# Optimization experiments

Measured on AMD Instinct MI355X. Metric: run time of the kernel, lower is better.

Reference implementation:

```python
import jax, jax.numpy as jnp
import numpy as np

EPS = 1e-6
ROPE_THETA = 10000.0


def setup_inputs() -> dict:
    key = jax.random.key(0)
    ks = jax.random.split(key, 6)
    B, S, D = 2, 2048, 2048
    H, KVH, HD = 16, 4, 128
    hidden_states = jax.random.normal(ks[0], (B, S, D), dtype=jnp.float32)
    # RoPE tables (HF style: freqs duplicated across the two halves)
    inv_freq = 1.0 / (ROPE_THETA ** (jnp.arange(0, HD, 2, dtype=jnp.float32) / HD))
    pos = jnp.arange(S, dtype=jnp.float32)
    freqs = pos[:, None] * inv_freq[None, :]            # [S, HD/2]
    emb = jnp.concatenate([freqs, freqs], axis=-1)       # [S, HD]
    cos, sin = jnp.cos(emb), jnp.sin(emb)
    w_scale = 0.02
    q_w = jax.random.normal(ks[1], (H * HD, D), dtype=jnp.float32) * w_scale
    k_w = jax.random.normal(ks[2], (KVH * HD, D), dtype=jnp.float32) * w_scale
    v_w = jax.random.normal(ks[3], (KVH * HD, D), dtype=jnp.float32) * w_scale
    o_w = jax.random.normal(ks[4], (D, H * HD), dtype=jnp.float32) * w_scale
    q_norm_w = jnp.ones((HD,), dtype=jnp.float32)
    k_norm_w = jnp.ones((HD,), dtype=jnp.float32)
    return {
        "hidden_states": hidden_states, "cos": cos, "sin": sin,
        "q_w": q_w, "k_w": k_w, "v_w": v_w, "o_w": o_w,
        "q_norm_w": q_norm_w, "k_norm_w": k_norm_w,
    }


def _rms_norm(x, w):
    # Qwen3RMSNorm: fp32 variance, scale, cast back
    xf = x.astype(jnp.float32)
    var = jnp.mean(xf * xf, axis=-1, keepdims=True)
    out = xf * jax.lax.rsqrt(var + EPS)
    return (out * w.astype(jnp.float32)).astype(x.dtype)


def _rotate_half(x):
    half = x.shape[-1] // 2
    return jnp.concatenate([-x[..., half:], x[..., :half]], axis=-1)


def reference(hidden_states, cos, sin, q_w, k_w, v_w, o_w, q_norm_w, k_norm_w):
    B, S, D = hidden_states.shape
    HD = q_norm_w.shape[0]
    H = q_w.shape[0] // HD
    KVH = k_w.shape[0] // HD
    groups = H // KVH
    scale = HD ** -0.5

    # QKV projections (no bias) -> [B, heads, S, HD]
    q = (hidden_states @ q_w.T).reshape(B, S, H, HD)
    k = (hidden_states @ k_w.T).reshape(B, S, KVH, HD)
    v = (hidden_states @ v_w.T).reshape(B, S, KVH, HD)
    q = _rms_norm(q, q_norm_w).transpose(0, 2, 1, 3)   # [B,H,S,HD]
    k = _rms_norm(k, k_norm_w).transpose(0, 2, 1, 3)   # [B,KVH,S,HD]
    v = v.transpose(0, 2, 1, 3)                        # [B,KVH,S,HD]

    # RoPE (broadcast over batch and heads)
    c = cos[None, None, :, :]
    s = sin[None, None, :, :]
    q = q * c + _rotate_half(q) * s
    k = k * c + _rotate_half(k) * s

    # GQA expand kv heads
    if groups > 1:
        k = jnp.repeat(k, groups, axis=1)              # [B,H,S,HD]
        v = jnp.repeat(v, groups, axis=1)

    # SDPA, non-causal, no mask, no dropout
    scores = jnp.einsum("bhqd,bhkd->bhqk", q, k) * scale
    probs = jax.nn.softmax(scores, axis=-1)
    attn = jnp.einsum("bhqk,bhkd->bhqd", probs, v)     # [B,H,S,HD]

    attn = attn.transpose(0, 2, 1, 3).reshape(B, S, H * HD)
    return attn @ o_w.T
```

## Files before the change

kernel.cpp:

```cpp
#include <hip/hip_runtime.h>
#include <hip/hip_bf16.h>
#include <math.h>

#define B_   2
#define S_   2048
#define D_   2048
#define H_   16
#define KVH_ 4
#define HD_  128
#define SCALE 0.08838834764831845f
#define LOG2E 1.44269504088896f

typedef unsigned short u16;
typedef unsigned int   u32;
typedef __attribute__((ext_vector_type(8)))  short bf16x8;
typedef __attribute__((ext_vector_type(4)))  float f32x4;
typedef __attribute__((ext_vector_type(16))) float f32x16;

__device__ __forceinline__ u16 f2bf(float x) {
    union { float f; unsigned int u; } v; v.f = x;
    unsigned int r = v.u + 0x7fffu + ((v.u >> 16) & 1u);
    return (u16)(r >> 16);
}
__device__ __forceinline__ float bf2f(u16 b) {
    union { float f; unsigned int u; } v; v.u = ((unsigned int)b) << 16;
    return v.f;
}
__device__ __forceinline__ u32 cvtpk(float lo, float hi) {
    u32 r;
    asm("v_cvt_pk_bf16_f32 %0, %1, %2" : "=v"(r) : "v"(lo), "v"(hi));
    return r;
}
__device__ __forceinline__ void gload16(const void* g, void* lds) {
    __builtin_amdgcn_global_load_lds(
        (const __attribute__((address_space(1))) unsigned int*)g,
        (__attribute__((address_space(3))) unsigned int*)lds, 16, 0, 0);
}

__global__ __launch_bounds__(256) void f2b_kernel(
    const float* __restrict__ s, u16* __restrict__ d, int n4)
{
    int i = blockIdx.x * 256 + threadIdx.x;
    if (i >= n4) return;
    float4 v = ((const float4*)s)[i];
    ushort4 o = make_ushort4(f2bf(v.x), f2bf(v.y), f2bf(v.z), f2bf(v.w));
    ((ushort4*)d)[i] = o;
}

template<int MODE>
__global__ __launch_bounds__(256) void gemm_bf16(
    const u16* __restrict__ A,
    const u16* __restrict__ Bw,
    u16* __restrict__ Qo, u16* __restrict__ Ko, u16* __restrict__ Vt,
    float* __restrict__ Co)
{
    __shared__ u16 As[128 * 64];
    __shared__ u16 Bs[128 * 64];

    const int t  = threadIdx.x;
    const int w  = t >> 6, l = t & 63;
    const int wm = w >> 1, wn = w & 1;
    const int lr = l & 15, lh = l >> 4;
    const int n0 = blockIdx.x * 128;
    const int m0 = blockIdx.y * 128;

    f32x4 acc[4][4];
    #pragma unroll
    for (int i = 0; i < 4; ++i)
        #pragma unroll
        for (int j = 0; j < 4; ++j)
            acc[i][j] = (f32x4)0.f;

    const int x  = (w * 4) * 1024 + l * 16;
    for (int k0 = 0; k0 < 2048; k0 += 64) {
        #pragma unroll
        for (int u = 0; u < 4; ++u) {
            int xb = x + u * 1024;
            int r  = xb >> 7;
            int c  = xb & 127;
            int cs = c ^ ((r & 7) << 4);
            gload16(&A[(size_t)(m0 + r) * 2048 + k0 + (cs >> 1)], &As[(w * 4 + u) * 512]);
            gload16(&Bw[(size_t)(n0 + r) * 2048 + k0 + (cs >> 1)], &Bs[(w * 4 + u) * 512]);
        }
        __syncthreads();
        #pragma unroll
        for (int kc = 0; kc < 2; ++kc) {
            bf16x8 af[4], bfr[4];
            #pragma unroll
            for (int i = 0; i < 4; ++i) {
                int row = wm * 64 + i * 16 + lr;
                int byt = row * 128 + ((kc * 64 + lh * 16) ^ ((row & 7) << 4));
                af[i] = *(const bf16x8*)&As[byt >> 1];
                int rob = wn * 64 + i * 16 + lr;
                int byb = rob * 128 + ((kc * 64 + lh * 16) ^ ((rob & 7) << 4));
                bfr[i] = *(const bf16x8*)&Bs[byb >> 1];
            }
            #pragma unroll
            for (int i = 0; i < 4; ++i)
                #pragma unroll
                for (int j = 0; j < 4; ++j)
                    acc[i][j] = __builtin_amdgcn_mfma_f32_16x16x32_bf16(
                        af[i], bfr[j], acc[i][j], 0, 0, 0);
        }
        __syncthreads();
    }

    #pragma unroll
    for (int i = 0; i < 4; ++i) {
        #pragma unroll
        for (int j = 0; j < 4; ++j) {
            int col = n0 + wn * 64 + j * 16 + lr;
            #pragma unroll
            for (int r = 0; r < 4; ++r) {
                int m = m0 + wm * 64 + i * 16 + lh * 4 + r;
                float v = acc[i][j][r];
                if (MODE == 0) {
                    int bb = m >> 11, s = m & 2047;
                    if (col < 2048) {
                        int hh = col >> 7, d = col & 127;
                        Qo[((size_t)(bb * H_ + hh) * S_ + s) * HD_ + d] = f2bf(v);
                    } else if (col < 2560) {
                        int c2 = col - 2048; int hh = c2 >> 7, d = c2 & 127;
                        Ko[((size_t)(bb * KVH_ + hh) * S_ + s) * HD_ + d] = f2bf(v);
                    } else {
                        int c2 = col - 2560; int hh = c2 >> 7, d = c2 & 127;
                        Vt[((size_t)(bb * KVH_ + hh) * HD_ + d) * S_ + s] = f2bf(v);
                    }
                } else {
                    Co[(size_t)m * 2048 + col] = v;
                }
            }
        }
    }
}

__global__ __launch_bounds__(256) void norm_rope(
    u16* __restrict__ Qb, u16* __restrict__ Kb,
    const float* __restrict__ cosb, const float* __restrict__ sinb,
    const float* __restrict__ qnw, const float* __restrict__ knw)
{
    const int rid = blockIdx.x * 4 + (threadIdx.x >> 6);
    const int l   = threadIdx.x & 63;
    u16* row; const float* wn; int s; float sc;
    if (rid < B_ * H_ * S_) {
        row = Qb + (size_t)rid * HD_; wn = qnw; s = rid & (S_ - 1); sc = SCALE * LOG2E;
    } else {
        int r2 = rid - B_ * H_ * S_;
        row = Kb + (size_t)r2 * HD_; wn = knw; s = r2 & (S_ - 1); sc = 1.f;
    }
    unsigned int u = *(const unsigned int*)&row[2 * l];
    float x0 = bf2f((u16)(u & 0xffff)), x1 = bf2f((u16)(u >> 16));
    float ss = x0 * x0 + x1 * x1;
    #pragma unroll
    for (int off = 1; off < 64; off <<= 1) ss += __shfl_xor(ss, off);
    float rr = rsqrtf(ss * (1.f / 128.f) + 1e-6f);
    float n0 = x0 * rr * wn[2 * l];
    float n1 = x1 * rr * wn[2 * l + 1];
    float p0 = __shfl_xor(n0, 32);
    float p1 = __shfl_xor(n1, 32);
    float sg = (l < 32) ? -1.f : 1.f;
    const float* cp = cosb + s * HD_;
    const float* sp = sinb + s * HD_;
    float o0 = (n0 * cp[2 * l]     + sg * p0 * sp[2 * l])     * sc;
    float o1 = (n1 * cp[2 * l + 1] + sg * p1 * sp[2 * l + 1]) * sc;
    unsigned int o = (unsigned int)f2bf(o0) | ((unsigned int)f2bf(o1) << 16);
    *(unsigned int*)&row[2 * l] = o;
}

__global__ __launch_bounds__(256, 2) void attn_mfma(
    const u16* __restrict__ Q,
    const u16* __restrict__ K,
    const u16* __restrict__ Vt,
    u16* __restrict__ AO)
{
    __shared__ u16 Ks[2][64 * 128];
    __shared__ u16 Vs[2][128 * 64];

    const int t  = threadIdx.x, w = t >> 6, l = t & 63;
    const int lq = l & 31, hi = l >> 5;
    const int id = (blockIdx.x & 7) * 64 + (blockIdx.x >> 3);
    const int qx = id & 15, bh = id >> 4;
    const int bb = bh >> 4, h = bh & 15;
    const int kv = bb * KVH_ + (h >> 2);
    const int q0 = qx * 128 + w * 32;

    const u16* Qp = Q + ((size_t)bh * S_ + q0) * HD_;
    const u16* Kp = K + (size_t)kv * S_ * HD_;
    const u16* Vp = Vt + (size_t)kv * HD_ * S_;

    bf16x8 aq[8];
    #pragma unroll
    for (int ks = 0; ks < 8; ++ks)
        aq[ks] = *(const bf16x8*)&Qp[(size_t)lq * 128 + ks * 16 + hi * 8];

    f32x16 oacc[4];
    #pragma unroll
    for (int dt = 0; dt < 4; ++dt) oacc[dt] = (f32x16)0.f;
    float mrun = -1e30f, lrun = 0.f;

    auto stage = [&](int k0, int buf) {
        #pragma unroll
        for (int u = 0; u < 4; ++u) {
            int xb = (w * 4 + u) * 1024 + l * 16;
            int rk = xb >> 8, ck = xb & 255;
            gload16(&Kp[(size_t)(k0 + rk) * 128 + ((ck ^ ((rk & 7) << 4)) >> 1)],
                    &Ks[buf][(w * 4 + u) * 512]);
            int rv = xb >> 7, cv = xb & 127;
            gload16(&Vp[(size_t)rv * S_ + k0 + ((cv ^ ((rv & 7) << 4)) >> 1)],
                    &Vs[buf][(w * 4 + u) * 512]);
        }
    };

    stage(0, 0);
    __syncthreads();

    const int NT = S_ / 64;
    for (int kt = 0; kt < NT; ++kt) {
        const int cur = kt & 1;
        if (kt + 1 < NT) stage((kt + 1) * 64, cur ^ 1);

        f32x16 sacc[2];
        sacc[0] = (f32x16)0.f; sacc[1] = (f32x16)0.f;
        #pragma unroll
        for (int kb = 0; kb < 2; ++kb) {
            #pragma unroll
            for (int ks = 0; ks < 8; ++ks) {
                int row = kb * 32 + lq;
                int byt = row * 256 + ((ks * 32 + hi * 16) ^ ((row & 7) << 4));
                bf16x8 kf = *(const bf16x8*)&Ks[cur][byt >> 1];
                sacc[kb] = __builtin_amdgcn_mfma_f32_32x32x16_bf16(
                    kf, aq[ks], sacc[kb], 0, 0, 0);
            }
        }

        float mx = -1e30f;
        #pragma unroll
        for (int kb = 0; kb < 2; ++kb)
            #pragma unroll
            for (int r = 0; r < 16; ++r)
                mx = fmaxf(mx, sacc[kb][r]);
        mx = fmaxf(mx, __shfl_xor(mx, 32));
        if (__any(mx > mrun + 8.f)) {
            float mn = fmaxf(mrun, mx);
            float al = __builtin_exp2f(mrun - mn);
            mrun = mn;
            lrun *= al;
            #pragma unroll
            for (int r = 0; r < 16; ++r) {
                int src = (r & 3) + 8 * (r >> 2) + 4 * hi;
                float alr = __shfl(al, src);
                #pragma unroll
                for (int dt = 0; dt < 4; ++dt) oacc[dt][r] *= alr;
            }
        }
        float ps = 0.f;
        #pragma unroll
        for (int kb = 0; kb < 2; ++kb)
            #pragma unroll
            for (int r = 0; r < 16; ++r) {
                float p = __builtin_exp2f(sacc[kb][r] - mrun);
                sacc[kb][r] = p;
                ps += p;
            }
        ps += __shfl_xor(ps, 32);
        lrun += ps;

        #pragma unroll
        for (int kb = 0; kb < 2; ++kb) {
            u32 wv[8], sv[8];
            #pragma unroll
            for (int i = 0; i < 8; ++i)
                wv[i] = cvtpk(sacc[kb][2 * i], sacc[kb][2 * i + 1]);
            #pragma unroll
            for (int i = 0; i < 8; ++i)
                sv[i] = __shfl_xor(wv[i], 32);
            #pragma unroll
            for (int k2 = 0; k2 < 2; ++k2) {
                union { u32 u[4]; bf16x8 v; } pa;
                pa.u[0] = hi ? sv[4 * k2 + 2] : wv[4 * k2 + 0];
                pa.u[1] = hi ? sv[4 * k2 + 3] : wv[4 * k2 + 1];
                pa.u[2] = hi ? wv[4 * k2 + 2] : sv[4 * k2 + 0];
                pa.u[3] = hi ? wv[4 * k2 + 3] : sv[4 * k2 + 1];
                int kloc = (kb * 2 + k2) * 16 + hi * 8;
                #pragma unroll
                for (int dt = 0; dt < 4; ++dt) {
                    int rowv = dt * 32 + lq;
                    int byv  = rowv * 128 + ((kloc * 2) ^ ((rowv & 7) << 4));
                    bf16x8 vf = *(const bf16x8*)&Vs[cur][byv >> 1];
                    oacc[dt] = __builtin_amdgcn_mfma_f32_32x32x16_bf16(
                        pa.v, vf, oacc[dt], 0, 0, 0);
                }
            }
        }
        __syncthreads();
    }

    #pragma unroll
    for (int r = 0; r < 16; ++r) {
        int src = (r & 3) + 8 * (r >> 2) + 4 * hi;
        float linv = 1.f / __shfl(lrun, src);
        int s = q0 + src;
        size_t base = ((size_t)bb * S_ + s) * 2048 + h * 128 + lq;
        #pragma unroll
        for (int dt = 0; dt < 4; ++dt)
            AO[base + dt * 32] = f2bf(oacc[dt][r] * linv);
    }
}

extern "C" void kernel_launch(void* const* d_in, const int* in_sizes, int n_in,
                              void* d_out, int out_size, void* d_ws, size_t ws_size,
                              hipStream_t stream) {
    (void)in_sizes; (void)n_in; (void)out_size; (void)ws_size;
    const float* hid  = (const float*)d_in[0];
    const float* cosb = (const float*)d_in[1];
    const float* sinb = (const float*)d_in[2];
    const float* qw   = (const float*)d_in[3];
    const float* kw   = (const float*)d_in[4];
    const float* vw   = (const float*)d_in[5];
    const float* ow   = (const float*)d_in[6];
    const float* qnw  = (const float*)d_in[7];
    const float* knw  = (const float*)d_in[8];

    u16* ws   = (u16*)d_ws;
    u16* hidB = ws;
    u16* Wc   = ws + 8388608;
    u16* owB  = ws + 14680064;
    u16* Qb   = ws + 18874368;
    u16* Kb   = ws + 27262976;
    u16* VtB  = ws + 29360128;
    u16* AO   = ws + 31457280;

    f2b_kernel<<<8192, 256, 0, stream>>>(hid, hidB, 2097152);
    f2b_kernel<<<4096, 256, 0, stream>>>(qw, Wc, 1048576);
    f2b_kernel<<<1024, 256, 0, stream>>>(kw, Wc + 4194304, 262144);
    f2b_kernel<<<1024, 256, 0, stream>>>(vw, Wc + 5242880, 262144);
    f2b_kernel<<<4096, 256, 0, stream>>>(ow, owB, 1048576);

    gemm_bf16<0><<<dim3(24, 32), 256, 0, stream>>>(hidB, Wc, Qb, Kb, VtB, nullptr);
    norm_rope<<<20480, 256, 0, stream>>>(Qb, Kb, cosb, sinb, qnw, knw);
    attn_mfma<<<512, 256, 0, stream>>>(Qb, Kb, VtB, AO);
    gemm_bf16<1><<<dim3(16, 32), 256, 0, stream>>>(AO, owB, nullptr, nullptr, nullptr,
                                                   (float*)d_out);
}
```

Measured before the change: 242.2 us.

## Fuse norm+RoPE into QKV GEMM epilogue, batch f32->bf16 casts, tune attention loop

Merges the five fp32-to-bf16 conversion launches into one 2D-grid kernel. Folds the per-head RMSNorm and RoPE into the QKV GEMM epilogue: each output tile is staged through padded LDS and one thread per row normalizes and rotates it, so the separate norm_rope pass with its read-modify-write of Q/K is gone. In attention, global K/V load addresses are precomputed and advanced by pointer increments, the loop is unrolled by 2, and s_setprio brackets the MFMA sections. The epilogue leaves only 128 of 256 threads working, with serial per-row loops and scattered cos/sin reads, which may slow the GEMM tail. The fused conversion grid also launches many idle blocks for the smaller tensors.

Result: slower. 294.0 us (+21.4%).

```diff
diff --git a/kernel.cpp b/kernel.cpp
--- a/kernel.cpp
+++ b/kernel.cpp
@@ -10,6 +10,7 @@
 #define HD_  128
 #define SCALE 0.08838834764831845f
 #define LOG2E 1.44269504088896f
+#define EPS_  1e-6f
 
 typedef unsigned short u16;
 typedef unsigned int   u32;
@@ -37,11 +38,23 @@
         (__attribute__((address_space(3))) unsigned int*)lds, 16, 0, 0);
 }
 
-__global__ __launch_bounds__(256) void f2b_kernel(
-    const float* __restrict__ s, u16* __restrict__ d, int n4)
+__global__ __launch_bounds__(256) void f2b_all(
+    const float* __restrict__ s0, u16* __restrict__ d0, int n0,
+    const float* __restrict__ s1, u16* __restrict__ d1, int n1,
+    const float* __restrict__ s2, u16* __restrict__ d2, int n2,
+    const float* __restrict__ s3, u16* __restrict__ d3, int n3,
+    const float* __restrict__ s4, u16* __restrict__ d4, int n4)
 {
+    const float* s; u16* d; int n;
+    switch (blockIdx.y) {
+        case 0: s = s0; d = d0; n = n0; break;
+        case 1: s = s1; d = d1; n = n1; break;
+        case 2: s = s2; d = d2; n = n2; break;
+        case 3: s = s3; d = d3; n = n3; break;
+        default: s = s4; d = d4; n = n4; break;
+    }
     int i = blockIdx.x * 256 + threadIdx.x;
-    if (i >= n4) return;
+    if (i >= n) return;
     float4 v = ((const float4*)s)[i];
     ushort4 o = make_ushort4(f2bf(v.x), f2bf(v.y), f2bf(v.z), f2bf(v.w));
     ((ushort4*)d)[i] = o;
@@ -52,10 +65,13 @@
     const u16* __restrict__ A,
     const u16* __restrict__ Bw,
     u16* __restrict__ Qo, u16* __restrict__ Ko, u16* __restrict__ Vt,
-    float* __restrict__ Co)
+    float* __restrict__ Co,
+    const float* __restrict__ cosb, const float* __restrict__ sinb,
+    const float* __restrict__ qnw, const float* __restrict__ knw)
 {
-    __shared__ u16 As[128 * 64];
-    __shared__ u16 Bs[128 * 64];
+    __shared__ u16 smem[17408];
+    u16* As = smem;
+    u16* Bs = smem + 8192;
 
     const int t  = threadIdx.x;
     const int w  = t >> 6, l = t & 63;
@@ -71,7 +87,7 @@
         for (int j = 0; j < 4; ++j)
             acc[i][j] = (f32x4)0.f;
 
-    const int x  = (w * 4) * 1024 + l * 16;
+    const int x = (w * 4) * 1024 + l * 16;
     for (int k0 = 0; k0 < 2048; k0 += 64) {
         #pragma unroll
         for (int u = 0; u < 4; ++u) {
@@ -105,66 +121,87 @@
         __syncthreads();
     }
 
-    #pragma unroll
-    for (int i = 0; i < 4; ++i) {
-        #pragma unroll
-        for (int j = 0; j < 4; ++j) {
-            int col = n0 + wn * 64 + j * 16 + lr;
-            #pragma unroll
-            for (int r = 0; r < 4; ++r) {
-                int m = m0 + wm * 64 + i * 16 + lh * 4 + r;
-                float v = acc[i][j][r];
-                if (MODE == 0) {
+    if (MODE == 1) {
+        #pragma unroll
+        for (int i = 0; i < 4; ++i)
+            #pragma unroll
+            for (int j = 0; j < 4; ++j) {
+                int col = n0 + wn * 64 + j * 16 + lr;
+                #pragma unroll
+                for (int r = 0; r < 4; ++r) {
+                    int m = m0 + wm * 64 + i * 16 + lh * 4 + r;
+                    Co[(size_t)m * 2048 + col] = acc[i][j][r];
+                }
+            }
+    } else if (n0 >= 2560) {
+        #pragma unroll
+        for (int i = 0; i < 4; ++i)
+            #pragma unroll
+            for (int j = 0; j < 4; ++j) {
+                int c2 = n0 - 2560 + wn * 64 + j * 16 + lr;
+                int hh = c2 >> 7, d = c2 & 127;
+                #pragma unroll
+                for (int r = 0; r < 4; ++r) {
+                    int m = m0 + wm * 64 + i * 16 + lh * 4 + r;
                     int bb = m >> 11, s = m & 2047;
-                    if (col < 2048) {
-                        int hh = col >> 7, d = col & 127;
-                        Qo[((size_t)(bb * H_ + hh) * S_ + s) * HD_ + d] = f2bf(v);
-                    } else if (col < 2560) {
-                        int c2 = col - 2048; int hh = c2 >> 7, d = c2 & 127;
-                        Ko[((size_t)(bb * KVH_ + hh) * S_ + s) * HD_ + d] = f2bf(v);
-                    } else {
-                        int c2 = col - 2560; int hh = c2 >> 7, d = c2 & 127;
-                        Vt[((size_t)(bb * KVH_ + hh) * HD_ + d) * S_ + s] = f2bf(v);
-                    }
-                } else {
-                    Co[(size_t)m * 2048 + col] = v;
-                }
-            }
-        }
-    }
-}
-
-__global__ __launch_bounds__(256) void norm_rope(
-    u16* __restrict__ Qb, u16* __restrict__ Kb,
-    const float* __restrict__ cosb, const float* __restrict__ sinb,
-    const float* __restrict__ qnw, const float* __restrict__ knw)
-{
-    const int rid = blockIdx.x * 4 + (threadIdx.x >> 6);
-    const int l   = threadIdx.x & 63;
-    u16* row; const float* wn; int s; float sc;
-    if (rid < B_ * H_ * S_) {
-        row = Qb + (size_t)rid * HD_; wn = qnw; s = rid & (S_ - 1); sc = SCALE * LOG2E;
+                    Vt[((size_t)(bb * KVH_ + hh) * HD_ + d) * S_ + s] =
+                        f2bf(acc[i][j][r]);
+                }
+            }
     } else {
-        int r2 = rid - B_ * H_ * S_;
-        row = Kb + (size_t)r2 * HD_; wn = knw; s = r2 & (S_ - 1); sc = 1.f;
-    }
-    unsigned int u = *(const unsigned int*)&row[2 * l];
-    float x0 = bf2f((u16)(u & 0xffff)), x1 = bf2f((u16)(u >> 16));
-    float ss = x0 * x0 + x1 * x1;
-    #pragma unroll
-    for (int off = 1; off < 64; off <<= 1) ss += __shfl_xor(ss, off);
-    float rr = rsqrtf(ss * (1.f / 128.f) + 1e-6f);
-    float n0 = x0 * rr * wn[2 * l];
-    float n1 = x1 * rr * wn[2 * l + 1];
-    float p0 = __shfl_xor(n0, 32);
-    float p1 = __shfl_xor(n1, 32);
-    float sg = (l < 32) ? -1.f : 1.f;
-    const float* cp = cosb + s * HD_;
-    const float* sp = sinb + s * HD_;
-    float o0 = (n0 * cp[2 * l]     + sg * p0 * sp[2 * l])     * sc;
-    float o1 = (n1 * cp[2 * l + 1] + sg * p1 * sp[2 * l + 1]) * sc;
-    unsigned int o = (unsigned int)f2bf(o0) | ((unsigned int)f2bf(o1) << 16);
-    *(unsigned int*)&row[2 * l] = o;
+        #pragma unroll
+        for (int i = 0; i < 4; ++i)
+            #pragma unroll
+            for (int j = 0; j < 4; ++j) {
+                int col = wn * 64 + j * 16 + lr;
+                #pragma unroll
+                for (int r = 0; r < 4; ++r) {
+                    int row = wm * 64 + i * 16 + lh * 4 + r;
+                    smem[row * 136 + col] = f2bf(acc[i][j][r]);
+                }
+            }
+        __syncthreads();
+        if (t < 128) {
+            const int row = t;
+            const int m   = m0 + row;
+            const int bb  = m >> 11, s = m & 2047;
+            const bool isQ = (n0 < 2048);
+            const int hh  = isQ ? (n0 >> 7) : ((n0 - 2048) >> 7);
+            const float* wnp = isQ ? qnw : knw;
+            const float scl  = isQ ? (SCALE * LOG2E) : 1.f;
+            const u16* cr = &smem[row * 136];
+            float ss = 0.f;
+            #pragma unroll
+            for (int kk = 0; kk < 16; ++kk) {
+                bf16x8 vv = *(const bf16x8*)&cr[kk * 8];
+                #pragma unroll
+                for (int e = 0; e < 8; ++e) {
+                    float xv = bf2f((u16)vv[e]); ss += xv * xv;
+                }
+            }
+            float rr = rsqrtf(ss * (1.f / 128.f) + EPS_);
+            u16* dst = isQ ? &Qo[((size_t)(bb * H_ + hh) * S_ + s) * HD_]
+                           : &Ko[((size_t)(bb * KVH_ + hh) * S_ + s) * HD_];
+            const float* cp = cosb + s * HD_;
+            const float* sp = sinb + s * HD_;
+            #pragma unroll
+            for (int kk = 0; kk < 8; ++kk) {
+                bf16x8 vlo = *(const bf16x8*)&cr[kk * 8];
+                bf16x8 vhi = *(const bf16x8*)&cr[64 + kk * 8];
+                union { u16 a[8]; bf16x8 v; } olo, ohi;
+                #pragma unroll
+                for (int e = 0; e < 8; ++e) {
+                    int d = kk * 8 + e;
+                    float nlo = bf2f((u16)vlo[e]) * rr * wnp[d];
+                    float nhi = bf2f((u16)vhi[e]) * rr * wnp[d + 64];
+                    olo.a[e] = f2bf((nlo * cp[d]      - nhi * sp[d])      * scl);
+                    ohi.a[e] = f2bf((nhi * cp[d + 64] + nlo * sp[d + 64]) * scl);
+                }
+                *(bf16x8*)&dst[kk * 8]      = olo.v;
+                *(bf16x8*)&dst[64 + kk * 8] = ohi.v;
+            }
+        }
+    }
 }
 
 __global__ __launch_bounds__(256, 2) void attn_mfma(
@@ -193,34 +230,44 @@
     for (int ks = 0; ks < 8; ++ks)
         aq[ks] = *(const bf16x8*)&Qp[(size_t)lq * 128 + ks * 16 + hi * 8];
 
+    const u16* kptr[4];
+    const u16* vptr[4];
+    #pragma unroll
+    for (int u = 0; u < 4; ++u) {
+        int xb = (w * 4 + u) * 1024 + l * 16;
+        int rk = xb >> 8, ck = xb & 255;
+        kptr[u] = &Kp[(size_t)rk * 128 + ((ck ^ ((rk & 7) << 4)) >> 1)];
+        int rv = xb >> 7, cv = xb & 127;
+        vptr[u] = &Vp[(size_t)rv * S_ + ((cv ^ ((rv & 7) << 4)) >> 1)];
+    }
+
     f32x16 oacc[4];
     #pragma unroll
     for (int dt = 0; dt < 4; ++dt) oacc[dt] = (f32x16)0.f;
     float mrun = -1e30f, lrun = 0.f;
 
-    auto stage = [&](int k0, int buf) {
+    auto stage = [&](int buf) {
         #pragma unroll
         for (int u = 0; u < 4; ++u) {
-            int xb = (w * 4 + u) * 1024 + l * 16;
-            int rk = xb >> 8, ck = xb & 255;
-            gload16(&Kp[(size_t)(k0 + rk) * 128 + ((ck ^ ((rk & 7) << 4)) >> 1)],
-                    &Ks[buf][(w * 4 + u) * 512]);
-            int rv = xb >> 7, cv = xb & 127;
-            gload16(&Vp[(size_t)rv * S_ + k0 + ((cv ^ ((rv & 7) << 4)) >> 1)],
-                    &Vs[buf][(w * 4 + u) * 512]);
+            gload16(kptr[u], &Ks[buf][(w * 4 + u) * 512]);
+            gload16(vptr[u], &Vs[buf][(w * 4 + u) * 512]);
+            kptr[u] += 64 * 128;
+            vptr[u] += 64;
         }
     };
 
-    stage(0, 0);
+    stage(0);
     __syncthreads();
 
     const int NT = S_ / 64;
+    #pragma unroll 2
     for (int kt = 0; kt < NT; ++kt) {
         const int cur = kt & 1;
-        if (kt + 1 < NT) stage((kt + 1) * 64, cur ^ 1);
+        if (kt + 1 < NT) stage(cur ^ 1);
 
         f32x16 sacc[2];
         sacc[0] = (f32x16)0.f; sacc[1] = (f32x16)0.f;
+        __builtin_amdgcn_s_setprio(1);
         #pragma unroll
         for (int kb = 0; kb < 2; ++kb) {
             #pragma unroll
@@ -232,13 +279,12 @@
                     kf, aq[ks], sacc[kb], 0, 0, 0);
             }
         }
+        __builtin_amdgcn_s_setprio(0);
 
         float mx = -1e30f;
         #pragma unroll
-        for (int kb = 0; kb < 2; ++kb)
-            #pragma unroll
-            for (int r = 0; r < 16; ++r)
-                mx = fmaxf(mx, sacc[kb][r]);
+        for (int r = 0; r < 16; ++r)
+            mx = fmaxf(mx, fmaxf(sacc[0][r], sacc[1][r]));
         mx = fmaxf(mx, __shfl_xor(mx, 32));
         if (__any(mx > mrun + 8.f)) {
             float mn = fmaxf(mrun, mx);
@@ -282,6 +328,7 @@
                 pa.u[2] = hi ? wv[4 * k2 + 2] : sv[4 * k2 + 0];
                 pa.u[3] = hi ? wv[4 * k2 + 3] : sv[4 * k2 + 1];
                 int kloc = (kb * 2 + k2) * 16 + hi * 8;
+                __builtin_amdgcn_s_setprio(1);
                 #pragma unroll
                 for (int dt = 0; dt < 4; ++dt) {
                     int rowv = dt * 32 + lq;
@@ -290,6 +337,7 @@
                     oacc[dt] = __builtin_amdgcn_mfma_f32_32x32x16_bf16(
                         pa.v, vf, oacc[dt], 0, 0, 0);
                 }
+                __builtin_amdgcn_s_setprio(0);
             }
         }
         __syncthreads();
@@ -330,15 +378,17 @@
     u16* VtB  = ws + 29360128;
     u16* AO   = ws + 31457280;
 
-    f2b_kernel<<<8192, 256, 0, stream>>>(hid, hidB, 2097152);
-    f2b_kernel<<<4096, 256, 0, stream>>>(qw, Wc, 1048576);
-    f2b_kernel<<<1024, 256, 0, stream>>>(kw, Wc + 4194304, 262144);
-    f2b_kernel<<<1024, 256, 0, stream>>>(vw, Wc + 5242880, 262144);
-    f2b_kernel<<<4096, 256, 0, stream>>>(ow, owB, 1048576);
-
-    gemm_bf16<0><<<dim3(24, 32), 256, 0, stream>>>(hidB, Wc, Qb, Kb, VtB, nullptr);
-    norm_rope<<<20480, 256, 0, stream>>>(Qb, Kb, cosb, sinb, qnw, knw);
+    f2b_all<<<dim3(8192, 5), 256, 0, stream>>>(
+        hid, hidB, 2097152,
+        qw,  Wc,            1048576,
+        kw,  Wc + 4194304,  262144,
+        vw,  Wc + 5242880,  262144,
+        ow,  owB,           1048576);
+
+    gemm_bf16<0><<<dim3(24, 32), 256, 0, stream>>>(
+        hidB, Wc, Qb, Kb, VtB, nullptr, cosb, sinb, qnw, knw);
     attn_mfma<<<512, 256, 0, stream>>>(Qb, Kb, VtB, AO);
-    gemm_bf16<1><<<dim3(16, 32), 256, 0, stream>>>(AO, owB, nullptr, nullptr, nullptr,
-                                                   (float*)d_out);
-}
+    gemm_bf16<1><<<dim3(16, 32), 256, 0, stream>>>(
+        AO, owB, nullptr, nullptr, nullptr, (float*)d_out,
+        nullptr, nullptr, nullptr, nullptr);
+}
```

## Merge conversion launches and tune attention loop with setprio and pointer increments

Applied to the files above, without the earlier changes.

Replaces the five separate fp32-to-bf16 conversion launches with one launch that selects the source by grid row, which removes per-launch overhead but launches idle blocks for the smaller tensors. In the attention kernel, K/V load addresses are precomputed once and advanced by pointer increments, the main loop is unrolled by two, and MFMA sections are wrapped in s_setprio to favour matrix issue across waves. The row-max reduction is also reshaped to interleave the two score tiles.

After: 243.0 us. Within noise of the previous version (+0.3%).

```diff
diff --git a/kernel.cpp b/kernel.cpp
--- a/kernel.cpp
+++ b/kernel.cpp
@@ -10,6 +10,7 @@
 #define HD_  128
 #define SCALE 0.08838834764831845f
 #define LOG2E 1.44269504088896f
+#define EPS_  1e-6f
 
 typedef unsigned short u16;
 typedef unsigned int   u32;
@@ -37,11 +38,23 @@
         (__attribute__((address_space(3))) unsigned int*)lds, 16, 0, 0);
 }
 
-__global__ __launch_bounds__(256) void f2b_kernel(
-    const float* __restrict__ s, u16* __restrict__ d, int n4)
+__global__ __launch_bounds__(256) void f2b_all(
+    const float* __restrict__ s0, u16* __restrict__ d0, int n0,
+    const float* __restrict__ s1, u16* __restrict__ d1, int n1,
+    const float* __restrict__ s2, u16* __restrict__ d2, int n2,
+    const float* __restrict__ s3, u16* __restrict__ d3, int n3,
+    const float* __restrict__ s4, u16* __restrict__ d4, int n4)
 {
+    const float* s; u16* d; int n;
+    switch (blockIdx.y) {
+        case 0: s = s0; d = d0; n = n0; break;
+        case 1: s = s1; d = d1; n = n1; break;
+        case 2: s = s2; d = d2; n = n2; break;
+        case 3: s = s3; d = d3; n = n3; break;
+        default: s = s4; d = d4; n = n4; break;
+    }
     int i = blockIdx.x * 256 + threadIdx.x;
-    if (i >= n4) return;
+    if (i >= n) return;
     float4 v = ((const float4*)s)[i];
     ushort4 o = make_ushort4(f2bf(v.x), f2bf(v.y), f2bf(v.z), f2bf(v.w));
     ((ushort4*)d)[i] = o;
@@ -71,7 +84,7 @@
         for (int j = 0; j < 4; ++j)
             acc[i][j] = (f32x4)0.f;
 
-    const int x  = (w * 4) * 1024 + l * 16;
+    const int x = (w * 4) * 1024 + l * 16;
     for (int k0 = 0; k0 < 2048; k0 += 64) {
         #pragma unroll
         for (int u = 0; u < 4; ++u) {
@@ -193,34 +206,44 @@
     for (int ks = 0; ks < 8; ++ks)
         aq[ks] = *(const bf16x8*)&Qp[(size_t)lq * 128 + ks * 16 + hi * 8];
 
+    const u16* kptr[4];
+    const u16* vptr[4];
+    #pragma unroll
+    for (int u = 0; u < 4; ++u) {
+        int xb = (w * 4 + u) * 1024 + l * 16;
+        int rk = xb >> 8, ck = xb & 255;
+        kptr[u] = &Kp[(size_t)rk * 128 + ((ck ^ ((rk & 7) << 4)) >> 1)];
+        int rv = xb >> 7, cv = xb & 127;
+        vptr[u] = &Vp[(size_t)rv * S_ + ((cv ^ ((rv & 7) << 4)) >> 1)];
+    }
+
     f32x16 oacc[4];
     #pragma unroll
     for (int dt = 0; dt < 4; ++dt) oacc[dt] = (f32x16)0.f;
     float mrun = -1e30f, lrun = 0.f;
 
-    auto stage = [&](int k0, int buf) {
+    auto stage = [&](int buf) {
         #pragma unroll
         for (int u = 0; u < 4; ++u) {
-            int xb = (w * 4 + u) * 1024 + l * 16;
-            int rk = xb >> 8, ck = xb & 255;
-            gload16(&Kp[(size_t)(k0 + rk) * 128 + ((ck ^ ((rk & 7) << 4)) >> 1)],
-                    &Ks[buf][(w * 4 + u) * 512]);
-            int rv = xb >> 7, cv = xb & 127;
-            gload16(&Vp[(size_t)rv * S_ + k0 + ((cv ^ ((rv & 7) << 4)) >> 1)],
-                    &Vs[buf][(w * 4 + u) * 512]);
+            gload16(kptr[u], &Ks[buf][(w * 4 + u) * 512]);
+            gload16(vptr[u], &Vs[buf][(w * 4 + u) * 512]);
+            kptr[u] += 64 * 128;
+            vptr[u] += 64;
         }
     };
 
-    stage(0, 0);
+    stage(0);
     __syncthreads();
 
     const int NT = S_ / 64;
+    #pragma unroll 2
     for (int kt = 0; kt < NT; ++kt) {
         const int cur = kt & 1;
-        if (kt + 1 < NT) stage((kt + 1) * 64, cur ^ 1);
+        if (kt + 1 < NT) stage(cur ^ 1);
 
         f32x16 sacc[2];
         sacc[0] = (f32x16)0.f; sacc[1] = (f32x16)0.f;
+        __builtin_amdgcn_s_setprio(1);
         #pragma unroll
         for (int kb = 0; kb < 2; ++kb) {
             #pragma unroll
@@ -232,13 +255,12 @@
                     kf, aq[ks], sacc[kb], 0, 0, 0);
             }
         }
+        __builtin_amdgcn_s_setprio(0);
 
         float mx = -1e30f;
         #pragma unroll
-        for (int kb = 0; kb < 2; ++kb)
-            #pragma unroll
-            for (int r = 0; r < 16; ++r)
-                mx = fmaxf(mx, sacc[kb][r]);
+        for (int r = 0; r < 16; ++r)
+            mx = fmaxf(mx, fmaxf(sacc[0][r], sacc[1][r]));
         mx = fmaxf(mx, __shfl_xor(mx, 32));
         if (__any(mx > mrun + 8.f)) {
             float mn = fmaxf(mrun, mx);
@@ -282,6 +304,7 @@
                 pa.u[2] = hi ? wv[4 * k2 + 2] : sv[4 * k2 + 0];
                 pa.u[3] = hi ? wv[4 * k2 + 3] : sv[4 * k2 + 1];
                 int kloc = (kb * 2 + k2) * 16 + hi * 8;
+                __builtin_amdgcn_s_setprio(1);
                 #pragma unroll
                 for (int dt = 0; dt < 4; ++dt) {
                     int rowv = dt * 32 + lq;
@@ -290,6 +313,7 @@
                     oacc[dt] = __builtin_amdgcn_mfma_f32_32x32x16_bf16(
                         pa.v, vf, oacc[dt], 0, 0, 0);
                 }
+                __builtin_amdgcn_s_setprio(0);
             }
         }
         __syncthreads();
@@ -330,11 +354,12 @@
     u16* VtB  = ws + 29360128;
     u16* AO   = ws + 31457280;
 
-    f2b_kernel<<<8192, 256, 0, stream>>>(hid, hidB, 2097152);
-    f2b_kernel<<<4096, 256, 0, stream>>>(qw, Wc, 1048576);
-    f2b_kernel<<<1024, 256, 0, stream>>>(kw, Wc + 4194304, 262144);
-    f2b_kernel<<<1024, 256, 0, stream>>>(vw, Wc + 5242880, 262144);
-    f2b_kernel<<<4096, 256, 0, stream>>>(ow, owB, 1048576);
+    f2b_all<<<dim3(8192, 5), 256, 0, stream>>>(
+        hid, hidB, 2097152,
+        qw,  Wc,            1048576,
+        kw,  Wc + 4194304,  262144,
+        vw,  Wc + 5242880,  262144,
+        ow,  owB,           1048576);
 
     gemm_bf16<0><<<dim3(24, 32), 256, 0, stream>>>(hidB, Wc, Qb, Kb, VtB, nullptr);
     norm_rope<<<20480, 256, 0, stream>>>(Qb, Kb, cosb, sinb, qnw, knw);
```
